# Performance work log

Measured on AMD Instinct MI355X. Metric: run time of the kernel, lower is better.

The kernel has to match this reference:

```python
import math
import jax, jax.numpy as jnp
import numpy as np

B, S, HID = 1, 2048, 2048
H, D = 32, 64            # heads, head_dim = HID // H
THETA = 10000.0
EPS = 1e-6
LAYER_IDX = 12
LAM_INIT = 0.8 - 0.6 * math.exp(-0.3 * LAYER_IDX)  # lambda_init_fn(layer_idx)
SCALE = 1.0 / math.sqrt(D)


def _rope_cos_sin(seq_len, dim):
    inv_freq = 1.0 / (THETA ** (np.arange(0, dim, 2, dtype=np.float64) / dim))
    freqs = np.outer(np.arange(seq_len, dtype=np.float64), inv_freq)
    emb = np.concatenate([freqs, freqs], axis=-1)  # [S, D] (llama duplicates freqs)
    return jnp.asarray(np.cos(emb), jnp.float32), jnp.asarray(np.sin(emb), jnp.float32)


def _rotate_half(x):
    return jnp.concatenate([-x[..., D // 2:], x[..., : D // 2]], axis=-1)


def _apply_rope(x, cos, sin):
    # x: [B, H, S, D]; cos/sin: [S, D] broadcast over B, H
    return x * cos + _rotate_half(x) * sin


def setup_inputs() -> dict:
    key = jax.random.key(0)
    ks = jax.random.split(key, 10)
    return {
        "hidden_states": jax.random.normal(ks[0], (B, S, HID), jnp.float32),
        "Wq": jax.random.normal(ks[1], (2 * HID, HID), jnp.float32) * 0.02,
        "Wk": jax.random.normal(ks[2], (2 * HID, HID), jnp.float32) * 0.02,
        "Wv": jax.random.normal(ks[3], (HID, HID), jnp.float32) * 0.02,
        "Wo": jax.random.normal(ks[4], (HID, HID), jnp.float32) * 0.02,
        "lambda_q1": jax.random.normal(ks[5], (D,), jnp.float32) * 0.1,
        "lambda_k1": jax.random.normal(ks[6], (D,), jnp.float32) * 0.1,
        "lambda_q2": jax.random.normal(ks[7], (D,), jnp.float32) * 0.1,
        "lambda_k2": jax.random.normal(ks[8], (D,), jnp.float32) * 0.1,
        "subln_w": jnp.ones((D,), jnp.float32),
    }


def reference(hidden_states, Wq, Wk, Wv, Wo,
              lambda_q1, lambda_k1, lambda_q2, lambda_k2, subln_w):
    # Projections (nn.Linear, no bias): x @ W.T
    q = hidden_states @ Wq.T                       # [B, S, 2*HID]
    k = hidden_states @ Wk.T                       # [B, S, 2*HID]
    v = hidden_states @ Wv.T                       # [B, S, HID]

    def to_heads(t):  # [B, S, H*D] -> [B, H, S, D]
        return t.reshape(B, S, H, D).transpose(0, 2, 1, 3)

    q1, q2 = jnp.split(q, 2, axis=-1)
    k1, k2 = jnp.split(k, 2, axis=-1)
    q1, q2, k1, k2, v = map(to_heads, (q1, q2, k1, k2, v))

    cos, sin = _rope_cos_sin(S, D)
    q1, k1 = _apply_rope(q1, cos, sin), _apply_rope(k1, cos, sin)
    q2, k2 = _apply_rope(q2, cos, sin), _apply_rope(k2, cos, sin)

    # Causal additive mask [S, S]
    causal = jnp.tril(jnp.ones((S, S), bool))
    neg_inf = jnp.finfo(jnp.float32).min
    mask = jnp.where(causal, 0.0, neg_inf)

    s1 = jnp.einsum("bhqd,bhkd->bhqk", q1, k1) * SCALE + mask
    s2 = jnp.einsum("bhqd,bhkd->bhqk", q2, k2) * SCALE + mask

    lam = (jnp.exp(jnp.sum(lambda_q1 * lambda_k1))
           - jnp.exp(jnp.sum(lambda_q2 * lambda_k2)) + LAM_INIT)

    attn_w = jax.nn.softmax(s1, axis=-1) - lam * jax.nn.softmax(s2, axis=-1)
    attn = jnp.einsum("bhqk,bhkd->bhqd", attn_w, v)  # [B, H, S, D]

    # Head-wise RMSNorm (LlamaRMSNorm over value_head_dim)
    var = jnp.mean(jnp.square(attn), axis=-1, keepdims=True)
    attn = attn * jax.lax.rsqrt(var + EPS) * subln_w
    attn = attn * (1.0 - LAM_INIT)

    out = attn.transpose(0, 2, 1, 3).reshape(B, S, HID) @ Wo.T
    return out
```

## Files before the change

### kernel.cpp

```cpp
#include <hip/hip_runtime.h>


typedef __bf16 bf16;
typedef __bf16 bf16x4 __attribute__((ext_vector_type(4)));
typedef __bf16 bf16x8 __attribute__((ext_vector_type(8)));
typedef float  f32x4  __attribute__((ext_vector_type(4)));
typedef unsigned int u32;
typedef u32 u32x2 __attribute__((ext_vector_type(2)));
typedef u32 u32x4 __attribute__((ext_vector_type(4)));

#define MFMA(a, b, c) __builtin_amdgcn_mfma_f32_16x16x32_bf16((a), (b), (c), 0, 0, 0)

#define S_LEN   2048
#define HID_DIM 2048
#define NHEAD   32
#define HD      64
#define QKV_N   10240
#define LAM_INIT 0.7836057665316245f
#define ONE_MINUS_LAM_INIT 0.21639423346837553f
#define QSCALE  0.18033688011112042f
#define RMS_EPS 1e-6f
#define L2T     0.4152410118609203f

__device__ __forceinline__ void gld16(const void* g, void* l) {
    __builtin_amdgcn_global_load_lds(
        (const __attribute__((address_space(1))) void*)g,
        (__attribute__((address_space(3))) void*)l, 16, 0, 0);
}

__device__ __forceinline__ void pa_build(u32 x, u32 y, int quad, u32& wlo, u32& whi) {
#if __has_builtin(__builtin_amdgcn_permlane32_swap) && __has_builtin(__builtin_amdgcn_permlane16_swap)
    u32x2 s = __builtin_amdgcn_permlane32_swap(x, y, false, false);
    u32x2 t = __builtin_amdgcn_permlane16_swap(s.x, s.y, false, false);
    wlo = t.x;
    whi = t.y;
#else
    const u32 x16 = (u32)__shfl_xor((int)x, 16, 64);
    const u32 x32 = (u32)__shfl_xor((int)x, 32, 64);
    const u32 x48 = (u32)__shfl_xor((int)x, 48, 64);
    const u32 y16 = (u32)__shfl_xor((int)y, 16, 64);
    const u32 y32 = (u32)__shfl_xor((int)y, 32, 64);
    const u32 y48 = (u32)__shfl_xor((int)y, 48, 64);
    wlo = (quad == 0) ? x   : (quad == 1) ? x48 : (quad == 2) ? y32 : y16;
    whi = (quad == 0) ? x16 : (quad == 1) ? x32 : (quad == 2) ? y48 : y;
#endif
}

__global__ void cvt_all(const float* __restrict__ hs, const float* __restrict__ Wq,
                        const float* __restrict__ Wk, const float* __restrict__ Wv,
                        const float* __restrict__ Wo,
                        const float* __restrict__ lq1, const float* __restrict__ lk1,
                        const float* __restrict__ lq2, const float* __restrict__ lk2,
                        bf16* __restrict__ hsb, bf16* __restrict__ Wb,
                        bf16* __restrict__ Wob, float* __restrict__ lam_out) {
    const int bid = blockIdx.x;
    if (bid >= 14336) {
        const int t = threadIdx.x;
        if (t < 64) {
            float a = lq1[t] * lk1[t];
            float b = lq2[t] * lk2[t];
            #pragma unroll
            for (int off = 32; off > 0; off >>= 1) {
                a += __shfl_xor(a, off, 64);
                b += __shfl_xor(b, off, 64);
            }
            if (t == 0) lam_out[0] = expf(a) - expf(b) + LAM_INIT;
        }
        return;
    }
    const float* src; bf16* dst; int off;
    if      (bid <  2048) { src = hs; dst = hsb;            off = bid;         }
    else if (bid <  6144) { src = Wq; dst = Wb;             off = bid - 2048;  }
    else if (bid < 10240) { src = Wk; dst = Wb +  8388608;  off = bid - 6144;  }
    else if (bid < 12288) { src = Wv; dst = Wb + 16777216;  off = bid - 10240; }
    else                  { src = Wo; dst = Wob;            off = bid - 12288; }
    const int i = off * 2048 + threadIdx.x * 8;
    float4 a = *(const float4*)(src + i);
    float4 b = *(const float4*)(src + i + 4);
    bf16x8 o = { (bf16)a.x, (bf16)a.y, (bf16)a.z, (bf16)a.w,
                 (bf16)b.x, (bf16)b.y, (bf16)b.z, (bf16)b.w };
    *(bf16x8*)(dst + i) = o;
}

__global__ __launch_bounds__(256, 4)
void qkv_rope_gemm(const bf16* __restrict__ A, const bf16* __restrict__ B,
                   bf16* __restrict__ Q1, bf16* __restrict__ Q2,
                   bf16* __restrict__ K1, bf16* __restrict__ K2,
                   bf16* __restrict__ Vt) {
    __shared__ __align__(16) bf16 As[128 * 64];
    __shared__ __align__(16) bf16 Bs[128 * 64];
    const int tid  = threadIdx.x;
    const int wave = tid >> 6, lane = tid & 63;
    const int wm = wave >> 1, wn = wave & 1;
    const int l = lane & 15, quad = lane >> 4;
    const int m0 = blockIdx.y * 128, n0 = blockIdx.x * 128;

    f32x4 acc[4][4];
    #pragma unroll
    for (int i = 0; i < 4; ++i)
        #pragma unroll
        for (int j = 0; j < 4; ++j) acc[i][j] = (f32x4){0.f, 0.f, 0.f, 0.f};

    const int rr  = tid >> 3;
    const int csw = ((tid & 7) ^ (rr & 7)) * 8;
    const bf16* Ag = A + (size_t)(m0 + rr) * HID_DIM + csw;
    const bf16* Bg = B + (size_t)(n0 + rr) * HID_DIM + csw;

    for (int kt = 0; kt < HID_DIM; kt += 64) {
        __syncthreads();
        #pragma unroll
        for (int j = 0; j < 4; ++j) {
            gld16(Ag + (size_t)(32 * j) * HID_DIM + kt, As + j * 2048 + tid * 8);
            gld16(Bg + (size_t)(32 * j) * HID_DIM + kt, Bs + j * 2048 + tid * 8);
        }
        __syncthreads();

        #pragma unroll
        for (int ks = 0; ks < 2; ++ks) {
            const int co = (((ks << 2) | quad) ^ (l & 7)) << 3;
            bf16x8 hf[4], wf[4];
            #pragma unroll
            for (int hi = 0; hi < 4; ++hi)
                hf[hi] = *(const bf16x8*)(As + (wm * 64 + hi * 16 + l) * 64 + co);
            #pragma unroll
            for (int wi = 0; wi < 4; ++wi)
                wf[wi] = *(const bf16x8*)(Bs + (wn * 64 + wi * 16 + l) * 64 + co);
            #pragma unroll
            for (int wi = 0; wi < 4; ++wi)
                #pragma unroll
                for (int hi = 0; hi < 4; ++hi)
                    acc[wi][hi] = MFMA(wf[wi], hf[hi], acc[wi][hi]);
        }
    }

    const int c = n0 + wn * 64;
    const int sbase = m0 + wm * 64;
    bf16* dst; int off; float scale = 1.0f; bool isv = false;
    if      (c < 2048) { dst = Q1; off = c;        scale = QSCALE; }
    else if (c < 4096) { dst = Q2; off = c - 2048; scale = QSCALE; }
    else if (c < 6144) { dst = K1; off = c - 4096; }
    else if (c < 8192) { dst = K2; off = c - 6144; }
    else               { isv = true; off = c - 8192; }
    const int h = off >> 6;

    if (!isv) {
        float invf[2][4];
        #pragma unroll
        for (int p = 0; p < 2; ++p)
            #pragma unroll
            for (int r = 0; r < 4; ++r)
                invf[p][r] = exp2f(-(float)(p * 16 + quad * 4 + r) * L2T);

        #pragma unroll
        for (int hi = 0; hi < 4; ++hi) {
            const float s = (float)(sbase + hi * 16 + l);
            float cs[2][4], sn[2][4];
            #pragma unroll
            for (int p = 0; p < 2; ++p)
                #pragma unroll
                for (int r = 0; r < 4; ++r) {
                    const float ang = s * invf[p][r];
                    cs[p][r] = __cosf(ang);
                    sn[p][r] = __sinf(ang);
                }
            bf16* rowp = dst + ((size_t)h * S_LEN + sbase + hi * 16 + l) * HD + quad * 4;
            #pragma unroll
            for (int wi = 0; wi < 4; ++wi) {
                const int p = wi & 1;
                const float sign = (wi < 2) ? -1.0f : 1.0f;
                bf16x4 o;
                #pragma unroll
                for (int r = 0; r < 4; ++r)
                    o[r] = (bf16)((acc[wi][hi][r] * cs[p][r] +
                                   sign * acc[wi ^ 2][hi][r] * sn[p][r]) * scale);
                *(bf16x4*)(rowp + wi * 16) = o;
            }
        }
    } else {
        #pragma unroll
        for (int wi = 0; wi < 4; ++wi)
            #pragma unroll
            for (int r = 0; r < 4; ++r) {
                bf16* vrow = Vt + ((size_t)h * HD + wi * 16 + quad * 4 + r) * S_LEN + sbase;
                #pragma unroll
                for (int hi = 0; hi < 4; ++hi)
                    vrow[hi * 16 + l] = (bf16)acc[wi][hi][r];
            }
    }
}

__global__ __launch_bounds__(256, 4)
void gemm_bt_splitk(const bf16* __restrict__ A, const bf16* __restrict__ B,
                    float* __restrict__ Cout, int M, int N, int K_total, int K_part) {
    __shared__ __align__(16) bf16 As[128 * 64];
    __shared__ __align__(16) bf16 Bs[128 * 64];
    const int tid  = threadIdx.x;
    const int wave = tid >> 6, lane = tid & 63;
    const int wm = wave >> 1, wn = wave & 1;
    const int l = lane & 15, quad = lane >> 4;
    const int m0 = blockIdx.y * 128, n0 = blockIdx.x * 128;
    const int kz = blockIdx.z * K_part;

    f32x4 acc[4][4];
    #pragma unroll
    for (int i = 0; i < 4; ++i)
        #pragma unroll
        for (int j = 0; j < 4; ++j) acc[i][j] = (f32x4){0.f, 0.f, 0.f, 0.f};

    const int rr  = tid >> 3;
    const int csw = ((tid & 7) ^ (rr & 7)) * 8;
    const bf16* Ag = A + (size_t)(m0 + rr) * K_total + kz + csw;
    const bf16* Bg = B + (size_t)(n0 + rr) * K_total + kz + csw;

    for (int kt = 0; kt < K_part; kt += 64) {
        __syncthreads();
        #pragma unroll
        for (int j = 0; j < 4; ++j) {
            gld16(Ag + (size_t)(32 * j) * K_total + kt, As + j * 2048 + tid * 8);
            gld16(Bg + (size_t)(32 * j) * K_total + kt, Bs + j * 2048 + tid * 8);
        }
        __syncthreads();

        #pragma unroll
        for (int ks = 0; ks < 2; ++ks) {
            const int co = (((ks << 2) | quad) ^ (l & 7)) << 3;
            bf16x8 af[4], bfr[4];
            #pragma unroll
            for (int mi = 0; mi < 4; ++mi)
                af[mi] = *(const bf16x8*)(As + (wm * 64 + mi * 16 + l) * 64 + co);
            #pragma unroll
            for (int ni = 0; ni < 4; ++ni)
                bfr[ni] = *(const bf16x8*)(Bs + (wn * 64 + ni * 16 + l) * 64 + co);
            #pragma unroll
            for (int mi = 0; mi < 4; ++mi)
                #pragma unroll
                for (int ni = 0; ni < 4; ++ni)
                    acc[mi][ni] = MFMA(af[mi], bfr[ni], acc[mi][ni]);
        }
    }

    float* Pf = Cout + (size_t)blockIdx.z * M * N;
    #pragma unroll
    for (int mi = 0; mi < 4; ++mi)
        #pragma unroll
        for (int ni = 0; ni < 4; ++ni)
            #pragma unroll
            for (int r = 0; r < 4; ++r) {
                const int row = m0 + wm * 64 + mi * 16 + quad * 4 + r;
                const int col = n0 + wn * 64 + ni * 16 + l;
                Pf[(size_t)row * N + col] = acc[mi][ni][r];
            }
}

__global__ void reduce_add(const float* __restrict__ p, float* __restrict__ out, int n) {
    const int i = (blockIdx.x * 256 + threadIdx.x) * 4;
    float4 a = *(const float4*)(p + i);
    float4 b = *(const float4*)(p + n + i);
    float4 o = { a.x + b.x, a.y + b.y, a.z + b.z, a.w + b.w };
    *(float4*)(out + i) = o;
}

__global__ __launch_bounds__(256, 3)
void diff_attn(const bf16* __restrict__ Q1, const bf16* __restrict__ K1,
               const bf16* __restrict__ Q2, const bf16* __restrict__ K2,
               const bf16* __restrict__ Vt, const float* __restrict__ lam_p,
               const float* __restrict__ subln_w, bf16* __restrict__ attn_out) {
    const int bid   = blockIdx.x;
    const int h     = (bid >> 1) & 31;
    const int qpair = bid >> 6;
    const int qb    = (bid & 1) ? qpair : (31 - qpair);
    const int q0    = qb * 64;
    const int tid  = threadIdx.x;
    const int wave = tid >> 6, lane = tid & 63;
    const int sid  = wave >> 1, ks = wave & 1;
    const int l    = lane & 15, quad = lane >> 4;

    __shared__ __align__(16) char smem[49152];

    const bf16* Qh  = (sid ? Q2 : Q1) + ((size_t)h * S_LEN + q0) * HD;
    const bf16* K1g = K1 + (size_t)h * S_LEN * HD;
    const bf16* K2g = K2 + (size_t)h * S_LEN * HD;
    const bf16* Vtg = Vt + (size_t)h * HD * S_LEN;

    const int rr  = tid >> 3;
    const int csw = ((tid & 7) ^ (rr & 7)) * 8;
    const int sw8 = l & 7;

    auto stage = [&](int kv, int bufb) {
        const bf16* k1p = K1g + (size_t)(kv + rr) * HD + csw;
        const bf16* k2p = K2g + (size_t)(kv + rr) * HD + csw;
        const bf16* vtp = Vtg + (size_t)rr * S_LEN + kv + csw;
        bf16* d1 = (bf16*)(smem + bufb)         + tid * 8;
        bf16* d2 = (bf16*)(smem + bufb + 8192)  + tid * 8;
        bf16* dv = (bf16*)(smem + bufb + 16384) + tid * 8;
        gld16(k1p,                       d1);
        gld16(k1p + (size_t)32 * HD,     d1 + 2048);
        gld16(k2p,                       d2);
        gld16(k2p + (size_t)32 * HD,     d2 + 2048);
        gld16(vtp,                       dv);
        gld16(vtp + (size_t)32 * S_LEN,  dv + 2048);
    };

    bf16x8 qf[4][2];
    #pragma unroll
    for (int g = 0; g < 4; ++g)
        #pragma unroll
        for (int dh = 0; dh < 2; ++dh)
            qf[g][dh] = *(const bf16x8*)(Qh + (g * 16 + l) * HD + dh * 32 + quad * 8);

    f32x4 O[4][4];
    #pragma unroll
    for (int g = 0; g < 4; ++g)
        #pragma unroll
        for (int nd = 0; nd < 4; ++nd)
            O[g][nd] = (f32x4){0.f, 0.f, 0.f, 0.f};
    float csum[4] = {0.f, 0.f, 0.f, 0.f};

    const int T = qb + 1;

    stage(0, 0);
    asm volatile("s_waitcnt vmcnt(0)" ::: "memory");
    __builtin_amdgcn_s_barrier();

    for (int t = 0; t < T; ++t) {
        const int bb = (t & 1) * 24576;
        if (t + 1 < T) stage((t + 1) * 64, 24576 - bb);

        {
            const bool diag = (t == qb);
            const bf16* Ksm = (const bf16*)(smem + bb + (sid ? 8192 : 0));
            const bf16* Vts = (const bf16*)(smem + bb + 16384);

            bf16x8 ka[2][2];
            #pragma unroll
            for (int mk = 0; mk < 2; ++mk) {
                const int krow = ((2 * ks + mk) * 16 + l) * 64;
                ka[mk][0] = *(const bf16x8*)(Ksm + krow + ((quad ^ sw8) << 3));
                ka[mk][1] = *(const bf16x8*)(Ksm + krow + (((4 + quad) ^ sw8) << 3));
            }
            bf16x8 vb[4];
            #pragma unroll
            for (int nd = 0; nd < 4; ++nd)
                vb[nd] = *(const bf16x8*)(Vts + (nd * 16 + l) * 64 +
                                          ((((ks << 2) + quad) ^ sw8) << 3));

            __builtin_amdgcn_s_setprio(1);
            #pragma unroll
            for (int g = 0; g < 4; ++g) {
                f32x4 c[2];
                #pragma unroll
                for (int mk = 0; mk < 2; ++mk) {
                    c[mk] = (f32x4){0.f, 0.f, 0.f, 0.f};
                    c[mk] = MFMA(ka[mk][0], qf[g][0], c[mk]);
                    c[mk] = MFMA(ka[mk][1], qf[g][1], c[mk]);
                }
                u32 dw[2][2];
                float lsum = 0.f;
                #pragma unroll
                for (int mk = 0; mk < 2; ++mk) {
                    float p[4];
                    #pragma unroll
                    for (int r = 0; r < 4; ++r) {
                        p[r] = __builtin_amdgcn_exp2f(c[mk][r]);
                        if (diag && ((2 * ks + mk) * 16 + quad * 4 + r > g * 16 + l))
                            p[r] = 0.f;
                        lsum += p[r];
                    }
                    asm("v_cvt_pk_bf16_f32 %0, %1, %2" : "=v"(dw[mk][0]) : "v"(p[0]), "v"(p[1]));
                    asm("v_cvt_pk_bf16_f32 %0, %1, %2" : "=v"(dw[mk][1]) : "v"(p[2]), "v"(p[3]));
                }
                csum[g] += lsum;

                u32 w0, w1, w2, w3;
                pa_build(dw[0][0], dw[1][0], quad, w0, w2);
                pa_build(dw[0][1], dw[1][1], quad, w1, w3);
                u32x4 wv = {w0, w1, w2, w3};
                bf16x8 pa;
                __builtin_memcpy(&pa, &wv, 16);

                #pragma unroll
                for (int nd = 0; nd < 4; ++nd)
                    O[g][nd] = MFMA(pa, vb[nd], O[g][nd]);
            }
            __builtin_amdgcn_s_setprio(0);
        }

        asm volatile("s_waitcnt vmcnt(0)" ::: "memory");
        __builtin_amdgcn_s_barrier();
    }

    __syncthreads();
    float* dO = (float*)(smem + sid * 17408);
    float* dC = (float*)(smem + 34816 + sid * 1024);
    if (ks == 1) {
        #pragma unroll
        for (int g = 0; g < 4; ++g)
            #pragma unroll
            for (int nd = 0; nd < 4; ++nd)
                *(f32x4*)(dO + lane * 68 + (g * 4 + nd) * 4) = O[g][nd];
        #pragma unroll
        for (int g = 0; g < 4; ++g) dC[g * 64 + lane] = csum[g];
    }
    __syncthreads();
    if (ks == 0) {
        #pragma unroll
        for (int g = 0; g < 4; ++g) {
            #pragma unroll
            for (int nd = 0; nd < 4; ++nd) {
                f32x4 o = *(const f32x4*)(dO + lane * 68 + (g * 4 + nd) * 4);
                O[g][nd] += o;
            }
            csum[g] += dC[g * 64 + lane];
        }
    }

    #pragma unroll
    for (int g = 0; g < 4; ++g) {
        csum[g] += __shfl_xor(csum[g], 16, 64);
        csum[g] += __shfl_xor(csum[g], 32, 64);
    }
    __syncthreads();

    float* epi = (float*)smem;

    if (sid == 1 && ks == 0) {
        const float lam = lam_p[0];
        #pragma unroll
        for (int mi = 0; mi < 4; ++mi)
            #pragma unroll
            for (int r = 0; r < 4; ++r) {
                const float inv = lam / __shfl(csum[mi], quad * 4 + r, 64);
                const int row = mi * 16 + quad * 4 + r;
                #pragma unroll
                for (int ni = 0; ni < 4; ++ni)
                    epi[row * 65 + ni * 16 + l] = O[mi][ni][r] * inv;
            }
    }
    __syncthreads();

    if (sid == 0 && ks == 0) {
        float sw[4];
        #pragma unroll
        for (int ni = 0; ni < 4; ++ni) sw[ni] = subln_w[ni * 16 + l];

        #pragma unroll
        for (int mi = 0; mi < 4; ++mi) {
            float inv1[4];
            #pragma unroll
            for (int r = 0; r < 4; ++r)
                inv1[r] = 1.0f / __shfl(csum[mi], quad * 4 + r, 64);

            float v[4][4]; float ssq[4] = {0.f, 0.f, 0.f, 0.f};
            #pragma unroll
            for (int ni = 0; ni < 4; ++ni)
                #pragma unroll
                for (int r = 0; r < 4; ++r) {
                    const int row = mi * 16 + quad * 4 + r;
                    const float x = O[mi][ni][r] * inv1[r] - epi[row * 65 + ni * 16 + l];
                    v[ni][r] = x;
                    ssq[r] += x * x;
                }
            #pragma unroll
            for (int r = 0; r < 4; ++r) {
                float s = ssq[r];
                s += __shfl_xor(s, 1, 64);
                s += __shfl_xor(s, 2, 64);
                s += __shfl_xor(s, 4, 64);
                s += __shfl_xor(s, 8, 64);
                ssq[r] = rsqrtf(s * (1.0f / 64.0f) + RMS_EPS) * ONE_MINUS_LAM_INIT;
            }
            #pragma unroll
            for (int ni = 0; ni < 4; ++ni)
                #pragma unroll
                for (int r = 0; r < 4; ++r) {
                    const int row = q0 + mi * 16 + quad * 4 + r;
                    attn_out[(size_t)row * HID_DIM + h * 64 + ni * 16 + l] =
                        (bf16)(v[ni][r] * ssq[r] * sw[ni]);
                }
        }
    }
}

extern "C" void kernel_launch(void* const* d_in, const int* in_sizes, int n_in,
                              void* d_out, int out_size, void* d_ws, size_t ws_size,
                              hipStream_t stream) {
    const float* hs  = (const float*)d_in[0];
    const float* Wq  = (const float*)d_in[1];
    const float* Wk  = (const float*)d_in[2];
    const float* Wv  = (const float*)d_in[3];
    const float* Wo  = (const float*)d_in[4];
    const float* lq1 = (const float*)d_in[5];
    const float* lk1 = (const float*)d_in[6];
    const float* lq2 = (const float*)d_in[7];
    const float* lk2 = (const float*)d_in[8];
    const float* slw = (const float*)d_in[9];

    if (ws_size < 151000000u) return;

    char* ws = (char*)d_ws;
    bf16*  hsb  = (bf16*)(ws);
    bf16*  Wb   = (bf16*)(ws + 8388608);
    bf16*  Wob  = (bf16*)(ws + 50331648);
    float* part = (float*)(ws + 58720256);
    bf16*  Q1b  = (bf16*)(ws + 100663296);
    bf16*  K1b  = (bf16*)(ws + 109051904);
    bf16*  Q2b  = (bf16*)(ws + 117440512);
    bf16*  K2b  = (bf16*)(ws + 125829120);
    bf16*  Vtb  = (bf16*)(ws + 134217728);
    bf16*  abuf = (bf16*)(ws + 142606336);
    float* lamp = (float*)(ws + 150994944);

    cvt_all<<<14337, 256, 0, stream>>>(hs, Wq, Wk, Wv, Wo, lq1, lk1, lq2, lk2,
                                       hsb, Wb, Wob, lamp);

    qkv_rope_gemm<<<dim3(QKV_N / 128, S_LEN / 128), 256, 0, stream>>>(
        hsb, Wb, Q1b, Q2b, K1b, K2b, Vtb);

    diff_attn<<<1024, 256, 0, stream>>>(Q1b, K1b, Q2b, K2b, Vtb, lamp, slw, abuf);

    gemm_bt_splitk<<<dim3(HID_DIM / 128, S_LEN / 128, 2), 256, 0, stream>>>(
        abuf, Wob, part, S_LEN, HID_DIM, HID_DIM, HID_DIM / 2);
    reduce_add<<<4096, 256, 0, stream>>>(part, (float*)d_out, S_LEN * HID_DIM);
}
```

Measured before the change: 384.1 us.

## Process 128-row query tiles with 512-thread blocks sharing K/V staging in attention

```diff
diff --git a/kernel.cpp b/kernel.cpp
--- a/kernel.cpp
+++ b/kernel.cpp
@@ -82,7 +82,7 @@
     *(bf16x8*)(dst + i) = o;
 }
 
-__global__ __launch_bounds__(256, 4)
+__global__ __launch_bounds__(256, 3)
 void qkv_rope_gemm(const bf16* __restrict__ A, const bf16* __restrict__ B,
                    bf16* __restrict__ Q1, bf16* __restrict__ Q2,
                    bf16* __restrict__ K1, bf16* __restrict__ K2,
@@ -189,7 +189,7 @@
     }
 }
 
-__global__ __launch_bounds__(256, 4)
+__global__ __launch_bounds__(256, 3)
 void gemm_bt_splitk(const bf16* __restrict__ A, const bf16* __restrict__ B,
                     float* __restrict__ Cout, int M, int N, int K_total, int K_part) {
     __shared__ __align__(16) bf16 As[128 * 64];
@@ -260,224 +260,222 @@
     *(float4*)(out + i) = o;
 }
 
-__global__ __launch_bounds__(256, 3)
+__global__ __launch_bounds__(512, 2)
 void diff_attn(const bf16* __restrict__ Q1, const bf16* __restrict__ K1,
                const bf16* __restrict__ Q2, const bf16* __restrict__ K2,
                const bf16* __restrict__ Vt, const float* __restrict__ lam_p,
                const float* __restrict__ subln_w, bf16* __restrict__ attn_out) {
-    const int bid   = blockIdx.x;
-    const int h     = (bid >> 1) & 31;
-    const int qpair = bid >> 6;
-    const int qb    = (bid & 1) ? qpair : (31 - qpair);
-    const int q0    = qb * 64;
+    const int bid  = blockIdx.x;
+    const int h    = bid & 31;
+    const int pp   = bid >> 5;
     const int tid  = threadIdx.x;
     const int wave = tid >> 6, lane = tid & 63;
-    const int sid  = wave >> 1, ks = wave & 1;
-    const int l    = lane & 15, quad = lane >> 4;
+    const int qhalf = wave >> 2, sid = (wave >> 1) & 1, ks = wave & 1;
+    const int l = lane & 15, quad = lane >> 4;
 
     __shared__ __align__(16) char smem[49152];
 
-    const bf16* Qh  = (sid ? Q2 : Q1) + ((size_t)h * S_LEN + q0) * HD;
     const bf16* K1g = K1 + (size_t)h * S_LEN * HD;
     const bf16* K2g = K2 + (size_t)h * S_LEN * HD;
     const bf16* Vtg = Vt + (size_t)h * HD * S_LEN;
+    const bf16* Qv  = (sid ? Q2 : Q1) + (size_t)h * S_LEN * HD;
 
     const int rr  = tid >> 3;
     const int csw = ((tid & 7) ^ (rr & 7)) * 8;
     const int sw8 = l & 7;
 
     auto stage = [&](int kv, int bufb) {
-        const bf16* k1p = K1g + (size_t)(kv + rr) * HD + csw;
-        const bf16* k2p = K2g + (size_t)(kv + rr) * HD + csw;
-        const bf16* vtp = Vtg + (size_t)rr * S_LEN + kv + csw;
-        bf16* d1 = (bf16*)(smem + bufb)         + tid * 8;
-        bf16* d2 = (bf16*)(smem + bufb + 8192)  + tid * 8;
-        bf16* dv = (bf16*)(smem + bufb + 16384) + tid * 8;
-        gld16(k1p,                       d1);
-        gld16(k1p + (size_t)32 * HD,     d1 + 2048);
-        gld16(k2p,                       d2);
-        gld16(k2p + (size_t)32 * HD,     d2 + 2048);
-        gld16(vtp,                       dv);
-        gld16(vtp + (size_t)32 * S_LEN,  dv + 2048);
+        gld16(K1g + (size_t)(kv + rr) * HD + csw,  (bf16*)(smem + bufb)         + tid * 8);
+        gld16(K2g + (size_t)(kv + rr) * HD + csw,  (bf16*)(smem + bufb + 8192)  + tid * 8);
+        gld16(Vtg + (size_t)rr * S_LEN + kv + csw, (bf16*)(smem + bufb + 16384) + tid * 8);
     };
 
-    bf16x8 qf[4][2];
-    #pragma unroll
-    for (int g = 0; g < 4; ++g)
-        #pragma unroll
-        for (int dh = 0; dh < 2; ++dh)
-            qf[g][dh] = *(const bf16x8*)(Qh + (g * 16 + l) * HD + dh * 32 + quad * 8);
-
-    f32x4 O[4][4];
-    #pragma unroll
-    for (int g = 0; g < 4; ++g)
-        #pragma unroll
-        for (int nd = 0; nd < 4; ++nd)
-            O[g][nd] = (f32x4){0.f, 0.f, 0.f, 0.f};
-    float csum[4] = {0.f, 0.f, 0.f, 0.f};
-
-    const int T = qb + 1;
-
-    stage(0, 0);
-    asm volatile("s_waitcnt vmcnt(0)" ::: "memory");
-    __builtin_amdgcn_s_barrier();
-
-    for (int t = 0; t < T; ++t) {
-        const int bb = (t & 1) * 24576;
-        if (t + 1 < T) stage((t + 1) * 64, 24576 - bb);
-
-        {
-            const bool diag = (t == qb);
-            const bf16* Ksm = (const bf16*)(smem + bb + (sid ? 8192 : 0));
-            const bf16* Vts = (const bf16*)(smem + bb + 16384);
-
-            bf16x8 ka[2][2];
-            #pragma unroll
-            for (int mk = 0; mk < 2; ++mk) {
-                const int krow = ((2 * ks + mk) * 16 + l) * 64;
-                ka[mk][0] = *(const bf16x8*)(Ksm + krow + ((quad ^ sw8) << 3));
-                ka[mk][1] = *(const bf16x8*)(Ksm + krow + (((4 + quad) ^ sw8) << 3));
-            }
-            bf16x8 vb[4];
+    for (int it = 0; it < 2; ++it) {
+        const int qb = it ? pp : (15 - pp);
+        const int q0 = qb * 128;
+        const bf16* Qh = Qv + (size_t)(q0 + qhalf * 64) * HD;
+
+        bf16x8 qf[4][2];
+        #pragma unroll
+        for (int g = 0; g < 4; ++g)
+            #pragma unroll
+            for (int dh = 0; dh < 2; ++dh)
+                qf[g][dh] = *(const bf16x8*)(Qh + (g * 16 + l) * HD + dh * 32 + quad * 8);
+
+        f32x4 O[4][4];
+        #pragma unroll
+        for (int g = 0; g < 4; ++g)
             #pragma unroll
             for (int nd = 0; nd < 4; ++nd)
-                vb[nd] = *(const bf16x8*)(Vts + (nd * 16 + l) * 64 +
-                                          ((((ks << 2) + quad) ^ sw8) << 3));
-
-            __builtin_amdgcn_s_setprio(1);
-            #pragma unroll
-            for (int g = 0; g < 4; ++g) {
-                f32x4 c[2];
-                #pragma unroll
-                for (int mk = 0; mk < 2; ++mk) {
-                    c[mk] = (f32x4){0.f, 0.f, 0.f, 0.f};
-                    c[mk] = MFMA(ka[mk][0], qf[g][0], c[mk]);
-                    c[mk] = MFMA(ka[mk][1], qf[g][1], c[mk]);
-                }
-                u32 dw[2][2];
-                float lsum = 0.f;
-                #pragma unroll
-                for (int mk = 0; mk < 2; ++mk) {
-                    float p[4];
-                    #pragma unroll
-                    for (int r = 0; r < 4; ++r) {
-                        p[r] = __builtin_amdgcn_exp2f(c[mk][r]);
-                        if (diag && ((2 * ks + mk) * 16 + quad * 4 + r > g * 16 + l))
-                            p[r] = 0.f;
-                        lsum += p[r];
-                    }
-                    asm("v_cvt_pk_bf16_f32 %0, %1, %2" : "=v"(dw[mk][0]) : "v"(p[0]), "v"(p[1]));
-                    asm("v_cvt_pk_bf16_f32 %0, %1, %2" : "=v"(dw[mk][1]) : "v"(p[2]), "v"(p[3]));
-                }
-                csum[g] += lsum;
-
-                u32 w0, w1, w2, w3;
-                pa_build(dw[0][0], dw[1][0], quad, w0, w2);
-                pa_build(dw[0][1], dw[1][1], quad, w1, w3);
-                u32x4 wv = {w0, w1, w2, w3};
-                bf16x8 pa;
-                __builtin_memcpy(&pa, &wv, 16);
-
-                #pragma unroll
-                for (int nd = 0; nd < 4; ++nd)
-                    O[g][nd] = MFMA(pa, vb[nd], O[g][nd]);
-            }
-            __builtin_amdgcn_s_setprio(0);
-        }
-
+                O[g][nd] = (f32x4){0.f, 0.f, 0.f, 0.f};
+        float csum[4] = {0.f, 0.f, 0.f, 0.f};
+
+        const int T  = 2 * qb + 2;
+        const int tq = 2 * qb + qhalf;
+
+        stage(0, 0);
         asm volatile("s_waitcnt vmcnt(0)" ::: "memory");
         __builtin_amdgcn_s_barrier();
-    }
-
-    __syncthreads();
-    float* dO = (float*)(smem + sid * 17408);
-    float* dC = (float*)(smem + 34816 + sid * 1024);
-    if (ks == 1) {
-        #pragma unroll
-        for (int g = 0; g < 4; ++g)
-            #pragma unroll
-            for (int nd = 0; nd < 4; ++nd)
-                *(f32x4*)(dO + lane * 68 + (g * 4 + nd) * 4) = O[g][nd];
-        #pragma unroll
-        for (int g = 0; g < 4; ++g) dC[g * 64 + lane] = csum[g];
-    }
-    __syncthreads();
-    if (ks == 0) {
+
+        for (int t = 0; t < T; ++t) {
+            const int bb = (t & 1) * 24576;
+            if (t + 1 < T) stage((t + 1) * 64, 24576 - bb);
+
+            if (t <= tq) {
+                const bool diag = (t == tq);
+                const bf16* Ksm = (const bf16*)(smem + bb + (sid ? 8192 : 0));
+                const bf16* Vts = (const bf16*)(smem + bb + 16384);
+
+                bf16x8 ka[2][2];
+                #pragma unroll
+                for (int mk = 0; mk < 2; ++mk) {
+                    const int krow = ((2 * ks + mk) * 16 + l) * 64;
+                    ka[mk][0] = *(const bf16x8*)(Ksm + krow + ((quad ^ sw8) << 3));
+                    ka[mk][1] = *(const bf16x8*)(Ksm + krow + (((4 + quad) ^ sw8) << 3));
+                }
+                bf16x8 vb[4];
+                #pragma unroll
+                for (int nd = 0; nd < 4; ++nd)
+                    vb[nd] = *(const bf16x8*)(Vts + (nd * 16 + l) * 64 +
+                                              ((((ks << 2) + quad) ^ sw8) << 3));
+
+                __builtin_amdgcn_s_setprio(1);
+                #pragma unroll
+                for (int g = 0; g < 4; ++g) {
+                    f32x4 c[2];
+                    #pragma unroll
+                    for (int mk = 0; mk < 2; ++mk) {
+                        c[mk] = (f32x4){0.f, 0.f, 0.f, 0.f};
+                        c[mk] = MFMA(ka[mk][0], qf[g][0], c[mk]);
+                        c[mk] = MFMA(ka[mk][1], qf[g][1], c[mk]);
+                    }
+                    u32 dw[2][2];
+                    float lsum = 0.f;
+                    #pragma unroll
+                    for (int mk = 0; mk < 2; ++mk) {
+                        float p[4];
+                        #pragma unroll
+                        for (int r = 0; r < 4; ++r) {
+                            p[r] = __builtin_amdgcn_exp2f(c[mk][r]);
+                            if (diag && ((2 * ks + mk) * 16 + quad * 4 + r > g * 16 + l))
+                                p[r] = 0.f;
+                            lsum += p[r];
+                        }
+                        asm("v_cvt_pk_bf16_f32 %0, %1, %2" : "=v"(dw[mk][0]) : "v"(p[0]), "v"(p[1]));
+                        asm("v_cvt_pk_bf16_f32 %0, %1, %2" : "=v"(dw[mk][1]) : "v"(p[2]), "v"(p[3]));
+                    }
+                    csum[g] += lsum;
+
+                    u32 w0, w1, w2, w3;
+                    pa_build(dw[0][0], dw[1][0], quad, w0, w2);
+                    pa_build(dw[0][1], dw[1][1], quad, w1, w3);
+                    u32x4 wv = {w0, w1, w2, w3};
+                    bf16x8 pa;
+                    __builtin_memcpy(&pa, &wv, 16);
+
+                    #pragma unroll
+                    for (int nd = 0; nd < 4; ++nd)
+                        O[g][nd] = MFMA(pa, vb[nd], O[g][nd]);
+                }
+                __builtin_amdgcn_s_setprio(0);
+            }
+
+            asm volatile("s_waitcnt vmcnt(0)" ::: "memory");
+            __builtin_amdgcn_s_barrier();
+        }
+
+        __syncthreads();
+        #pragma unroll
+        for (int round = 0; round < 2; ++round) {
+            float* dO = (float*)(smem + sid * 17408);
+            float* dC = (float*)(smem + 34816 + sid * 1024);
+            if (qhalf == round && ks == 1) {
+                #pragma unroll
+                for (int g = 0; g < 4; ++g)
+                    #pragma unroll
+                    for (int nd = 0; nd < 4; ++nd)
+                        *(f32x4*)(dO + lane * 68 + (g * 4 + nd) * 4) = O[g][nd];
+                #pragma unroll
+                for (int g = 0; g < 4; ++g) dC[g * 64 + lane] = csum[g];
+            }
+            __syncthreads();
+            if (qhalf == round && ks == 0) {
+                #pragma unroll
+                for (int g = 0; g < 4; ++g) {
+                    #pragma unroll
+                    for (int nd = 0; nd < 4; ++nd)
+                        O[g][nd] += *(const f32x4*)(dO + lane * 68 + (g * 4 + nd) * 4);
+                    csum[g] += dC[g * 64 + lane];
+                }
+            }
+            __syncthreads();
+        }
+
         #pragma unroll
         for (int g = 0; g < 4; ++g) {
-            #pragma unroll
-            for (int nd = 0; nd < 4; ++nd) {
-                f32x4 o = *(const f32x4*)(dO + lane * 68 + (g * 4 + nd) * 4);
-                O[g][nd] += o;
-            }
-            csum[g] += dC[g * 64 + lane];
-        }
-    }
-
-    #pragma unroll
-    for (int g = 0; g < 4; ++g) {
-        csum[g] += __shfl_xor(csum[g], 16, 64);
-        csum[g] += __shfl_xor(csum[g], 32, 64);
-    }
-    __syncthreads();
-
-    float* epi = (float*)smem;
-
-    if (sid == 1 && ks == 0) {
-        const float lam = lam_p[0];
-        #pragma unroll
-        for (int mi = 0; mi < 4; ++mi)
-            #pragma unroll
-            for (int r = 0; r < 4; ++r) {
-                const float inv = lam / __shfl(csum[mi], quad * 4 + r, 64);
-                const int row = mi * 16 + quad * 4 + r;
+            csum[g] += __shfl_xor(csum[g], 16, 64);
+            csum[g] += __shfl_xor(csum[g], 32, 64);
+        }
+
+        float* epi = (float*)smem;
+
+        if (sid == 1 && ks == 0) {
+            const float lam = lam_p[0];
+            #pragma unroll
+            for (int mi = 0; mi < 4; ++mi)
+                #pragma unroll
+                for (int r = 0; r < 4; ++r) {
+                    const float inv = lam / __shfl(csum[mi], quad * 4 + r, 64);
+                    const int row = qhalf * 64 + mi * 16 + quad * 4 + r;
+                    #pragma unroll
+                    for (int ni = 0; ni < 4; ++ni)
+                        epi[row * 65 + ni * 16 + l] = O[mi][ni][r] * inv;
+                }
+        }
+        __syncthreads();
+
+        if (sid == 0 && ks == 0) {
+            float sw[4];
+            #pragma unroll
+            for (int ni = 0; ni < 4; ++ni) sw[ni] = subln_w[ni * 16 + l];
+
+            #pragma unroll
+            for (int mi = 0; mi < 4; ++mi) {
+                float inv1[4];
+                #pragma unroll
+                for (int r = 0; r < 4; ++r)
+                    inv1[r] = 1.0f / __shfl(csum[mi], quad * 4 + r, 64);
+
+                float v[4][4]; float ssq[4] = {0.f, 0.f, 0.f, 0.f};
                 #pragma unroll
                 for (int ni = 0; ni < 4; ++ni)
-                    epi[row * 65 + ni * 16 + l] = O[mi][ni][r] * inv;
-            }
-    }
-    __syncthreads();
-
-    if (sid == 0 && ks == 0) {
-        float sw[4];
-        #pragma unroll
-        for (int ni = 0; ni < 4; ++ni) sw[ni] = subln_w[ni * 16 + l];
-
-        #pragma unroll
-        for (int mi = 0; mi < 4; ++mi) {
-            float inv1[4];
-            #pragma unroll
-            for (int r = 0; r < 4; ++r)
-                inv1[r] = 1.0f / __shfl(csum[mi], quad * 4 + r, 64);
-
-            float v[4][4]; float ssq[4] = {0.f, 0.f, 0.f, 0.f};
-            #pragma unroll
-            for (int ni = 0; ni < 4; ++ni)
+                    #pragma unroll
+                    for (int r = 0; r < 4; ++r) {
+                        const int row = qhalf * 64 + mi * 16 + quad * 4 + r;
+                        const float x = O[mi][ni][r] * inv1[r] - epi[row * 65 + ni * 16 + l];
+                        v[ni][r] = x;
+                        ssq[r] += x * x;
+                    }
                 #pragma unroll
                 for (int r = 0; r < 4; ++r) {
-                    const int row = mi * 16 + quad * 4 + r;
-                    const float x = O[mi][ni][r] * inv1[r] - epi[row * 65 + ni * 16 + l];
-                    v[ni][r] = x;
-                    ssq[r] += x * x;
+                    float s = ssq[r];
+                    s += __shfl_xor(s, 1, 64);
+                    s += __shfl_xor(s, 2, 64);
+                    s += __shfl_xor(s, 4, 64);
+                    s += __shfl_xor(s, 8, 64);
+                    ssq[r] = rsqrtf(s * (1.0f / 64.0f) + RMS_EPS) * ONE_MINUS_LAM_INIT;
                 }
-            #pragma unroll
-            for (int r = 0; r < 4; ++r) {
-                float s = ssq[r];
-                s += __shfl_xor(s, 1, 64);
-                s += __shfl_xor(s, 2, 64);
-                s += __shfl_xor(s, 4, 64);
-                s += __shfl_xor(s, 8, 64);
-                ssq[r] = rsqrtf(s * (1.0f / 64.0f) + RMS_EPS) * ONE_MINUS_LAM_INIT;
-            }
-            #pragma unroll
-            for (int ni = 0; ni < 4; ++ni)
-                #pragma unroll
-                for (int r = 0; r < 4; ++r) {
-                    const int row = q0 + mi * 16 + quad * 4 + r;
-                    attn_out[(size_t)row * HID_DIM + h * 64 + ni * 16 + l] =
-                        (bf16)(v[ni][r] * ssq[r] * sw[ni]);
-                }
-        }
+                #pragma unroll
+                for (int ni = 0; ni < 4; ++ni)
+                    #pragma unroll
+                    for (int r = 0; r < 4; ++r) {
+                        const int row = q0 + qhalf * 64 + mi * 16 + quad * 4 + r;
+                        attn_out[(size_t)row * HID_DIM + h * 64 + ni * 16 + l] =
+                            (bf16)(v[ni][r] * ssq[r] * sw[ni]);
+                    }
+            }
+        }
+        __syncthreads();
     }
 }
 
@@ -516,7 +514,7 @@
     qkv_rope_gemm<<<dim3(QKV_N / 128, S_LEN / 128), 256, 0, stream>>>(
         hsb, Wb, Q1b, Q2b, K1b, K2b, Vtb);
 
-    diff_attn<<<1024, 256, 0, stream>>>(Q1b, K1b, Q2b, K2b, Vtb, lamp, slw, abuf);
+    diff_attn<<<256, 512, 0, stream>>>(Q1b, K1b, Q2b, K2b, Vtb, lamp, slw, abuf);
 
     gemm_bt_splitk<<<dim3(HID_DIM / 128, S_LEN / 128, 2), 256, 0, stream>>>(
         abuf, Wob, part, S_LEN, HID_DIM, HID_DIM, HID_DIM / 2);
```

After: 343.8 us. 10.5% less time.
